# Kernel tuning notes

Measured on AMD Instinct MI355X. Metric: run time of the kernel, lower is better.

Reference implementation:

```python
import jax, jax.numpy as jnp
import numpy as np
from jax import lax

IOU_THRESHOLD = 0.5
CONF_THRESHOLD = 0.05
MAX_DETECTIONS = 100


def setup_inputs() -> dict:
    key = jax.random.key(0)
    k1, k2, k3 = jax.random.split(key, 3)
    B, N, C = 8, 100000, 80
    # xyxy boxes: top-left in [0,64), size in [16,128)
    xy = jax.random.uniform(k1, (B, N, 2), dtype=jnp.float32) * 64.0
    wh = jax.random.uniform(k2, (B, N, 2), dtype=jnp.float32) * 112.0 + 16.0
    box_prediction = jnp.concatenate([xy, xy + wh], axis=-1)
    # class logits (from_logits=True); scale so max softmax prob clears threshold
    class_prediction = jax.random.normal(k3, (B, N, C), dtype=jnp.float32) * 2.0
    return {"box_prediction": box_prediction, "class_prediction": class_prediction}


def _iou_one_vs_all(ref, boxes):
    # tf.image.non_max_suppression semantics: coords treated as corners
    # [a, b, c, d]; area = (c-a)*(d-b); iou=0 if either area <= 0.
    a_r, b_r, c_r, d_r = ref[0], ref[1], ref[2], ref[3]
    area_r = (c_r - a_r) * (d_r - b_r)
    area_b = (boxes[:, 2] - boxes[:, 0]) * (boxes[:, 3] - boxes[:, 1])
    ih = jnp.maximum(0.0, jnp.minimum(c_r, boxes[:, 2]) - jnp.maximum(a_r, boxes[:, 0]))
    iw = jnp.maximum(0.0, jnp.minimum(d_r, boxes[:, 3]) - jnp.maximum(b_r, boxes[:, 1]))
    inter = ih * iw
    union = area_r + area_b - inter
    ok = (area_r > 0) & (area_b > 0) & (union > 0)
    return jnp.where(ok, inter / jnp.where(ok, union, 1.0), 0.0)


def _nms_one(boxes, scores):
    # greedy NMS on a single image: boxes [N,4], scores [N]
    active0 = scores >= CONF_THRESHOLD

    def step(active, _):
        masked = jnp.where(active, scores, -jnp.inf)
        idx = jnp.argmax(masked)
        ok = active[idx]
        iou = _iou_one_vs_all(boxes[idx], boxes)
        active = active & (iou <= IOU_THRESHOLD)
        active = active.at[idx].set(False)
        return active, (idx, ok)

    _, (idxs, oks) = lax.scan(step, active0, None, length=MAX_DETECTIONS)
    return idxs, oks  # [M] int, [M] bool


def _forward(box_prediction, class_prediction):
    # convert_format xyxy -> xywh (x, y, w, h)
    x1, y1, x2, y2 = jnp.split(box_prediction, 4, axis=-1)
    boxes = jnp.concatenate([x1, y1, x2 - x1, y2 - y1], axis=-1)  # [B,N,4]
    cls_p = jax.nn.softmax(class_prediction, axis=-1)  # from_logits=True
    scores = jnp.max(cls_p, axis=-1)  # [B,N]
    idxs, oks = jax.vmap(_nms_one)(boxes, scores)  # [B,M], [B,M]
    boxes_sel = jnp.take_along_axis(boxes, idxs[:, :, None], axis=1)  # [B,M,4]
    cls_sel = jnp.take_along_axis(cls_p, idxs[:, :, None], axis=1)  # [B,M,C]
    boxes_out = jnp.where(oks[:, :, None], boxes_sel, 0.0)
    cls_out = jnp.where(oks[:, :, None], cls_sel, 0.0)
    return boxes_out, cls_out


def reference(box_prediction, class_prediction):
    boxes_out, cls_out = _forward(box_prediction, class_prediction)
    cls_idx = jnp.argmax(cls_out, axis=2)
    return boxes_out, cls_idx, cls_out
```

## Files before the change

kernel.cpp:

```cpp
#include <hip/hip_runtime.h>
#include <stdint.h>

#define BATCH 8
#define NCLS 80
#define MAXDET 100
#define CAP 512
#define NBINS 10240
#define TT 1024
#define TCHUNK 10
#define BASEKEY (0x3D4CCCCDu >> 12)

__global__ __launch_bounds__(256)
void scores_kernel(const float* __restrict__ cls,
                   float* __restrict__ scores, int BN) {
  int gid = blockIdx.x * 256 + threadIdx.x;
  int row = gid >> 1;
  int l = gid & 1;
  if (row >= BN) return;
  const float4* p4 = (const float4*)(cls + (size_t)row * NCLS);

  float4 v[10];
#pragma unroll
  for (int i = 0; i < 10; i++) v[i] = p4[l + 2 * i];

  float m = fmaxf(fmaxf(v[0].x, v[0].y), fmaxf(v[0].z, v[0].w));
#pragma unroll
  for (int i = 1; i < 10; i++)
    m = fmaxf(m, fmaxf(fmaxf(v[i].x, v[i].y), fmaxf(v[i].z, v[i].w)));
  m = fmaxf(m, __shfl_xor(m, 1));

  float a0 = 0.f, a1 = 0.f, a2 = 0.f, a3 = 0.f;
#pragma unroll
  for (int i = 0; i < 10; i++) {
    a0 += expf(v[i].x - m);
    a1 += expf(v[i].y - m);
    a2 += expf(v[i].z - m);
    a3 += expf(v[i].w - m);
  }
  float s_half = (a0 + a1) + (a2 + a3);
  float s = s_half + __shfl_xor(s_half, 1);
  if (l == 0) scores[row] = 1.0f / s;
}

__global__ __launch_bounds__(TT)
void tail_kernel(const float* __restrict__ box, const float* __restrict__ cls,
                 const float* __restrict__ scores,
                 float* __restrict__ out, int N) {
  __shared__ uint32_t lh[NBINS];
  __shared__ uint32_t chs[TT];
  __shared__ unsigned long long sk[CAP];
  __shared__ float sbox[CAP][4];
  __shared__ uint32_t sidx[CAP];
  __shared__ float4 accb[MAXDET];
  __shared__ float4 accp[MAXDET];
  __shared__ uint32_t pick_i[MAXDET];
  __shared__ int T_sh, nacc_sh;
  __shared__ uint32_t lctr;

  const int b = blockIdx.x;
  const int tid = threadIdx.x;
  const float* sc = scores + (size_t)b * N;

#pragma unroll
  for (int j = 0; j < TCHUNK; j++) lh[tid + j * TT] = 0;
  if (tid < CAP) sk[tid] = 0ULL;
  if (tid == 0) { lctr = 0; T_sh = NBINS; }
  __syncthreads();

  const float4* sc4 = (const float4*)sc;
  const int N4 = N >> 2;
  for (int i = tid; i < N4; i += TT) {
    float4 v = sc4[i];
    if (v.x >= 0.05f) atomicAdd(&lh[(__float_as_uint(v.x) >> 12) - BASEKEY], 1u);
    if (v.y >= 0.05f) atomicAdd(&lh[(__float_as_uint(v.y) >> 12) - BASEKEY], 1u);
    if (v.z >= 0.05f) atomicAdd(&lh[(__float_as_uint(v.z) >> 12) - BASEKEY], 1u);
    if (v.w >= 0.05f) atomicAdd(&lh[(__float_as_uint(v.w) >> 12) - BASEKEY], 1u);
  }
  for (int i = (N4 << 2) + tid; i < N; i += TT) {
    float s = sc[i];
    if (s >= 0.05f) atomicAdd(&lh[(__float_as_uint(s) >> 12) - BASEKEY], 1u);
  }
  __syncthreads();

  uint32_t csum = 0;
#pragma unroll
  for (int j = 0; j < TCHUNK; j++) csum += lh[tid * TCHUNK + j];
  chs[tid] = csum;
  __syncthreads();
  for (int off = 1; off < TT; off <<= 1) {
    uint32_t v = chs[tid];
    uint32_t add = (tid + off < TT) ? chs[tid + off] : 0u;
    __syncthreads();
    chs[tid] = v + add;
    __syncthreads();
  }
  {
    uint32_t St = chs[tid];
    uint32_t Sprev = (tid > 0) ? chs[tid - 1] : 0xFFFFFFFFu;
    if (St <= CAP && (tid == 0 || Sprev > CAP)) {
      int T = 0;
      if (tid != 0) {
        uint32_t cum = St;
        int lo = (tid - 1) * TCHUNK;
        T = lo;
        for (int bb = tid * TCHUNK - 1; bb >= lo; bb--) {
          uint32_t nb = cum + lh[bb];
          if (nb > CAP) { T = bb + 1; break; }
          cum = nb;
          if (bb == lo) T = lo;
        }
      }
      T_sh = T;
    }
  }
  __syncthreads();
  const uint32_t T = (uint32_t)T_sh;

  for (int i = tid; i < N4; i += TT) {
    float4 v = sc4[i];
#pragma unroll
    for (int c = 0; c < 4; c++) {
      float s = (c == 0) ? v.x : (c == 1) ? v.y : (c == 2) ? v.z : v.w;
      if (s >= 0.05f) {
        uint32_t key = (__float_as_uint(s) >> 12) - BASEKEY;
        if (key >= T) {
          uint32_t slot = atomicAdd(&lctr, 1u);
          if (slot < CAP)
            sk[slot] = ((unsigned long long)__float_as_uint(s) << 32) |
                       (unsigned long long)(~(uint32_t)(i * 4 + c));
        }
      }
    }
  }
  for (int i = (N4 << 2) + tid; i < N; i += TT) {
    float s = sc[i];
    if (s >= 0.05f) {
      uint32_t key = (__float_as_uint(s) >> 12) - BASEKEY;
      if (key >= T) {
        uint32_t slot = atomicAdd(&lctr, 1u);
        if (slot < CAP)
          sk[slot] = ((unsigned long long)__float_as_uint(s) << 32) |
                     (unsigned long long)(~(uint32_t)i);
      }
    }
  }
  __syncthreads();
  uint32_t nc = lctr; if (nc > CAP) nc = CAP;

  for (int k = 2; k <= CAP; k <<= 1) {
    for (int j = k >> 1; j > 0; j >>= 1) {
      int i = tid;
      if (i < CAP) {
        int ixj = i ^ j;
        if (ixj > i) {
          unsigned long long a = sk[i], c = sk[ixj];
          if (((i & k) == 0) ? (a < c) : (a > c)) { sk[i] = c; sk[ixj] = a; }
        }
      }
      __syncthreads();
    }
  }

  if (tid < CAP) {
    unsigned long long k = sk[tid];
    uint32_t idx = (uint32_t)k ^ 0xFFFFFFFFu;
    sidx[tid] = idx;
    if (k != 0ULL) {
      const float4 f = *(const float4*)(box + ((size_t)b * N + idx) * 4);
      sbox[tid][0] = f.x; sbox[tid][1] = f.y;
      sbox[tid][2] = f.z - f.x; sbox[tid][3] = f.w - f.y;
    } else {
      sbox[tid][0] = 0.f; sbox[tid][1] = 0.f; sbox[tid][2] = 0.f; sbox[tid][3] = 0.f;
    }
  }
  __syncthreads();

  if (tid < 64) {
    const int lane = tid;
    int nacc = 0, nprop = 0;
    for (int cursor = 0; cursor < (int)nc && nacc < MAXDET; cursor += 64) {
      const int c = cursor + lane;
      bool alive = (c < (int)nc);
      float c0 = 0.f, c1 = 0.f, c2 = 0.f, c3 = 0.f;
      uint32_t myidx = 0;
      if (alive) {
        c0 = sbox[c][0]; c1 = sbox[c][1]; c2 = sbox[c][2]; c3 = sbox[c][3];
        myidx = sidx[c];
      }
      const float area_b = (c2 - c0) * (c3 - c1);

#pragma unroll 2
      for (int a = 0; a < nprop; a++) {
        float4 ar = accp[a];
        float area_r = (ar.z - ar.x) * (ar.w - ar.y);
        float ih = fmaxf(0.f, fminf(ar.z, c2) - fmaxf(ar.x, c0));
        float iw = fmaxf(0.f, fminf(ar.w, c3) - fmaxf(ar.y, c1));
        float inter = ih * iw;
        float uni = area_r + area_b - inter;
        bool okk = (area_r > 0.f) && (area_b > 0.f) && (uni > 0.f);
        float iou = okk ? (inter / uni) : 0.f;
        if (iou > 0.5f) alive = false;
      }

      unsigned long long am = __ballot(alive);
      while (am != 0ULL && nacc < MAXDET) {
        int L = (int)(__ffsll(am) - 1);
        float r0 = __shfl(c0, L), r1 = __shfl(c1, L);
        float r2 = __shfl(c2, L), r3 = __shfl(c3, L);
        uint32_t ridx = (uint32_t)__shfl((int)myidx, L);
        bool proper = (r2 > r0) && (r3 > r1);
        if (lane == 0) {
          pick_i[nacc] = ridx;
          accb[nacc] = make_float4(r0, r1, r2, r3);
          if (proper) accp[nprop] = make_float4(r0, r1, r2, r3);
        }
        asm volatile("s_waitcnt lgkmcnt(0)" ::: "memory");
        if (lane == L) alive = false;
        if (proper) {
          if (alive) {
            float area_r = (r2 - r0) * (r3 - r1);
            float ih = fmaxf(0.f, fminf(r2, c2) - fmaxf(r0, c0));
            float iw = fmaxf(0.f, fminf(r3, c3) - fmaxf(r1, c1));
            float inter = ih * iw;
            float uni = area_r + area_b - inter;
            bool okk = (area_r > 0.f) && (area_b > 0.f) && (uni > 0.f);
            float iou = okk ? (inter / uni) : 0.f;
            if (iou > 0.5f) alive = false;
          }
          nprop++;
        }
        am = __ballot(alive);
        nacc++;
      }
    }
    if (lane == 0) nacc_sh = nacc;
  }
  __syncthreads();

  const int nacc = nacc_sh;
  if (tid >= MAXDET) return;
  const int r = b * MAXDET + tid;
  float* boxes_out  = out;
  float* clsidx_out = out + BATCH * MAXDET * 4;
  float* cls_out    = out + BATCH * MAXDET * 4 + BATCH * MAXDET;

  if (tid >= nacc) {
    boxes_out[r * 4 + 0] = 0.f; boxes_out[r * 4 + 1] = 0.f;
    boxes_out[r * 4 + 2] = 0.f; boxes_out[r * 4 + 3] = 0.f;
    clsidx_out[r] = 0.f;
    for (int j = 0; j < NCLS; j++) cls_out[r * NCLS + j] = 0.f;
    return;
  }
  float4 bb = accb[tid];
  boxes_out[r * 4 + 0] = bb.x;
  boxes_out[r * 4 + 1] = bb.y;
  boxes_out[r * 4 + 2] = bb.z;
  boxes_out[r * 4 + 3] = bb.w;

  uint32_t idx = pick_i[tid];
  const float4* p = (const float4*)(cls + ((size_t)b * N + idx) * NCLS);
  float x[NCLS];
#pragma unroll
  for (int i = 0; i < NCLS / 4; i++) {
    float4 v = p[i];
    x[4 * i] = v.x; x[4 * i + 1] = v.y; x[4 * i + 2] = v.z; x[4 * i + 3] = v.w;
  }
  float m = x[0];
#pragma unroll
  for (int i = 1; i < NCLS; i++) m = fmaxf(m, x[i]);
  float r8[8];
#pragma unroll
  for (int j = 0; j < 8; j++) r8[j] = 0.0f;
#pragma unroll
  for (int i = 0; i < NCLS / 8; i++)
#pragma unroll
    for (int j = 0; j < 8; j++) r8[j] += expf(x[i * 8 + j] - m);
  float s = ((r8[0] + r8[1]) + (r8[2] + r8[3])) + ((r8[4] + r8[5]) + (r8[6] + r8[7]));

  float best = -1.f; int bi = 0;
  for (int j = 0; j < NCLS; j++) {
    float pj = expf(x[j] - m) / s;
    cls_out[r * NCLS + j] = pj;
    if (pj > best) { best = pj; bi = j; }
  }
  clsidx_out[r] = (float)bi;
}

extern "C" void kernel_launch(void* const* d_in, const int* in_sizes, int n_in,
                              void* d_out, int out_size, void* d_ws, size_t ws_size,
                              hipStream_t stream) {
  (void)n_in; (void)out_size; (void)ws_size;
  const float* box = (const float*)d_in[0];
  const float* cls = (const float*)d_in[1];
  const int N = in_sizes[0] / (BATCH * 4);
  const int BN = BATCH * N;

  float* ws_scores = (float*)d_ws;

  {
    long long tot = (long long)BN * 2;
    int blocks = (int)((tot + 255) / 256);
    scores_kernel<<<blocks, 256, 0, stream>>>(cls, ws_scores, BN);
  }
  tail_kernel<<<BATCH, TT, 0, stream>>>(box, cls, ws_scores, (float*)d_out, N);
}
```

Measured before the change: 116.8 us.

## Stage class logits through LDS with coalesced wave loads in persistent scores kernel

```diff
diff --git a/kernel.cpp b/kernel.cpp
--- a/kernel.cpp
+++ b/kernel.cpp
@@ -10,36 +10,71 @@
 #define TCHUNK 10
 #define BASEKEY (0x3D4CCCCDu >> 12)
 
+#define SG_ROWS 32
+#define SG_PAD 84
+#define SG_WAVES 4
+#define SG_BLOCKS 768
+
 __global__ __launch_bounds__(256)
 void scores_kernel(const float* __restrict__ cls,
                    float* __restrict__ scores, int BN) {
-  int gid = blockIdx.x * 256 + threadIdx.x;
-  int row = gid >> 1;
-  int l = gid & 1;
-  if (row >= BN) return;
-  const float4* p4 = (const float4*)(cls + (size_t)row * NCLS);
-
-  float4 v[10];
-#pragma unroll
-  for (int i = 0; i < 10; i++) v[i] = p4[l + 2 * i];
-
-  float m = fmaxf(fmaxf(v[0].x, v[0].y), fmaxf(v[0].z, v[0].w));
-#pragma unroll
-  for (int i = 1; i < 10; i++)
-    m = fmaxf(m, fmaxf(fmaxf(v[i].x, v[i].y), fmaxf(v[i].z, v[i].w)));
-  m = fmaxf(m, __shfl_xor(m, 1));
-
-  float a0 = 0.f, a1 = 0.f, a2 = 0.f, a3 = 0.f;
-#pragma unroll
-  for (int i = 0; i < 10; i++) {
-    a0 += expf(v[i].x - m);
-    a1 += expf(v[i].y - m);
-    a2 += expf(v[i].z - m);
-    a3 += expf(v[i].w - m);
-  }
-  float s_half = (a0 + a1) + (a2 + a3);
-  float s = s_half + __shfl_xor(s_half, 1);
-  if (l == 0) scores[row] = 1.0f / s;
+  __shared__ float slab_all[SG_WAVES * SG_ROWS * SG_PAD];
+  const int lane = threadIdx.x & 63;
+  const int wid  = threadIdx.x >> 6;
+  float* slab = slab_all + wid * (SG_ROWS * SG_PAD);
+  const int ngroups = (BN + SG_ROWS - 1) / SG_ROWS;
+  const int wstride = gridDim.x * SG_WAVES;
+
+  for (int g = blockIdx.x * SG_WAVES + wid; g < ngroups; g += wstride) {
+    const int row0 = g * SG_ROWS;
+    int rows = BN - row0; if (rows > SG_ROWS) rows = SG_ROWS;
+    const int nf4 = rows * 20;
+    const float4* src = (const float4*)(cls + (size_t)row0 * NCLS);
+
+    float4 vr[10];
+#pragma unroll
+    for (int k = 0; k < 10; k++) {
+      int f = k * 64 + lane;
+      if (f < nf4) vr[k] = src[f];
+    }
+#pragma unroll
+    for (int k = 0; k < 10; k++) {
+      int f = k * 64 + lane;
+      if (f < nf4) {
+        int r = f / 20, p = f - r * 20;
+        *(float4*)&slab[r * SG_PAD + p * 4] = vr[k];
+      }
+    }
+    asm volatile("s_waitcnt lgkmcnt(0)" ::: "memory");
+
+    const int rt = lane >> 1;
+    const int l = lane & 1;
+    if (rt < rows) {
+      const float4* t4 = (const float4*)&slab[rt * SG_PAD];
+      float4 v[10];
+#pragma unroll
+      for (int i = 0; i < 10; i++) v[i] = t4[l + 2 * i];
+
+      float m = fmaxf(fmaxf(v[0].x, v[0].y), fmaxf(v[0].z, v[0].w));
+#pragma unroll
+      for (int i = 1; i < 10; i++)
+        m = fmaxf(m, fmaxf(fmaxf(v[i].x, v[i].y), fmaxf(v[i].z, v[i].w)));
+      m = fmaxf(m, __shfl_xor(m, 1));
+
+      float a0 = 0.f, a1 = 0.f, a2 = 0.f, a3 = 0.f;
+#pragma unroll
+      for (int i = 0; i < 10; i++) {
+        a0 += expf(v[i].x - m);
+        a1 += expf(v[i].y - m);
+        a2 += expf(v[i].z - m);
+        a3 += expf(v[i].w - m);
+      }
+      float s_half = (a0 + a1) + (a2 + a3);
+      float s = s_half + __shfl_xor(s_half, 1);
+      if (l == 0) scores[row0 + rt] = 1.0f / s;
+    }
+    asm volatile("s_waitcnt lgkmcnt(0)" ::: "memory");
+  }
 }
 
 __global__ __launch_bounds__(TT)
@@ -297,10 +332,6 @@
 
   float* ws_scores = (float*)d_ws;
 
-  {
-    long long tot = (long long)BN * 2;
-    int blocks = (int)((tot + 255) / 256);
-    scores_kernel<<<blocks, 256, 0, stream>>>(cls, ws_scores, BN);
-  }
+  scores_kernel<<<SG_BLOCKS, 256, 0, stream>>>(cls, ws_scores, BN);
   tail_kernel<<<BATCH, TT, 0, stream>>>(box, cls, ws_scores, (float*)d_out, N);
 }
```

New measurement: 223.3 us. 1.91x slower.

## Stage softmax-score rows through double-buffered LDS with persistent waves

Applied to the files above, without the earlier changes.

```diff
diff --git a/kernel.cpp b/kernel.cpp
--- a/kernel.cpp
+++ b/kernel.cpp
@@ -10,36 +10,91 @@
 #define TCHUNK 10
 #define BASEKEY (0x3D4CCCCDu >> 12)
 
-__global__ __launch_bounds__(256)
+#define PR_ROWS 32
+#define PR_PAD 84
+#define PR_WAVES 2
+#define PR_BLOCKS 768
+
+__global__ __launch_bounds__(128, 1)
 void scores_kernel(const float* __restrict__ cls,
                    float* __restrict__ scores, int BN) {
-  int gid = blockIdx.x * 256 + threadIdx.x;
-  int row = gid >> 1;
-  int l = gid & 1;
-  if (row >= BN) return;
-  const float4* p4 = (const float4*)(cls + (size_t)row * NCLS);
-
-  float4 v[10];
-#pragma unroll
-  for (int i = 0; i < 10; i++) v[i] = p4[l + 2 * i];
-
-  float m = fmaxf(fmaxf(v[0].x, v[0].y), fmaxf(v[0].z, v[0].w));
-#pragma unroll
-  for (int i = 1; i < 10; i++)
-    m = fmaxf(m, fmaxf(fmaxf(v[i].x, v[i].y), fmaxf(v[i].z, v[i].w)));
-  m = fmaxf(m, __shfl_xor(m, 1));
-
-  float a0 = 0.f, a1 = 0.f, a2 = 0.f, a3 = 0.f;
-#pragma unroll
-  for (int i = 0; i < 10; i++) {
-    a0 += expf(v[i].x - m);
-    a1 += expf(v[i].y - m);
-    a2 += expf(v[i].z - m);
-    a3 += expf(v[i].w - m);
-  }
-  float s_half = (a0 + a1) + (a2 + a3);
-  float s = s_half + __shfl_xor(s_half, 1);
-  if (l == 0) scores[row] = 1.0f / s;
+  __shared__ float slab_all[PR_WAVES * 2 * PR_ROWS * PR_PAD];
+  const int lane = threadIdx.x & 63;
+  const int wid  = threadIdx.x >> 6;
+  float* slabA = slab_all + (wid * 2 + 0) * (PR_ROWS * PR_PAD);
+  float* slabB = slab_all + (wid * 2 + 1) * (PR_ROWS * PR_PAD);
+  const int ngroups = (BN + PR_ROWS - 1) / PR_ROWS;
+  const int wstride = gridDim.x * PR_WAVES;
+
+  int g = blockIdx.x * PR_WAVES + wid;
+  if (g >= ngroups) return;
+
+  int rr[10], pp[10];
+#pragma unroll
+  for (int k = 0; k < 10; k++) {
+    int f = k * 64 + lane;
+    rr[k] = f / 20; pp[k] = (f - rr[k] * 20) * 4;
+  }
+
+  {
+    const float4* src = (const float4*)(cls + (size_t)g * PR_ROWS * NCLS);
+    float4 st[10];
+#pragma unroll
+    for (int k = 0; k < 10; k++) st[k] = src[k * 64 + lane];
+#pragma unroll
+    for (int k = 0; k < 10; k++) *(float4*)&slabA[rr[k] * PR_PAD + pp[k]] = st[k];
+  }
+
+  int cur = 0;
+  while (true) {
+    const int gn = g + wstride;
+
+    float4 st[10];
+    const bool have_next = (gn < ngroups);
+    if (have_next) {
+      const float4* srcn = (const float4*)(cls + (size_t)gn * PR_ROWS * NCLS);
+#pragma unroll
+      for (int k = 0; k < 10; k++) st[k] = srcn[k * 64 + lane];
+    }
+
+    {
+      float* slab = cur ? slabB : slabA;
+      const int rt = lane >> 1;
+      const int l = lane & 1;
+      const float4* t4 = (const float4*)&slab[rt * PR_PAD];
+      float4 v[10];
+#pragma unroll
+      for (int i = 0; i < 10; i++) v[i] = t4[l + 2 * i];
+
+      float m = fmaxf(fmaxf(v[0].x, v[0].y), fmaxf(v[0].z, v[0].w));
+#pragma unroll
+      for (int i = 1; i < 10; i++)
+        m = fmaxf(m, fmaxf(fmaxf(v[i].x, v[i].y), fmaxf(v[i].z, v[i].w)));
+      m = fmaxf(m, __shfl_xor(m, 1));
+
+      float a0 = 0.f, a1 = 0.f, a2 = 0.f, a3 = 0.f;
+#pragma unroll
+      for (int i = 0; i < 10; i++) {
+        a0 += expf(v[i].x - m);
+        a1 += expf(v[i].y - m);
+        a2 += expf(v[i].z - m);
+        a3 += expf(v[i].w - m);
+      }
+      float s_half = (a0 + a1) + (a2 + a3);
+      float s = s_half + __shfl_xor(s_half, 1);
+      if (l == 0) scores[g * PR_ROWS + rt] = 1.0f / s;
+    }
+
+    if (!have_next) break;
+
+    {
+      float* sl = cur ? slabA : slabB;
+#pragma unroll
+      for (int k = 0; k < 10; k++) *(float4*)&sl[rr[k] * PR_PAD + pp[k]] = st[k];
+    }
+    cur ^= 1;
+    g = gn;
+  }
 }
 
 __global__ __launch_bounds__(TT)
@@ -297,10 +352,6 @@
 
   float* ws_scores = (float*)d_ws;
 
-  {
-    long long tot = (long long)BN * 2;
-    int blocks = (int)((tot + 255) / 256);
-    scores_kernel<<<blocks, 256, 0, stream>>>(cls, ws_scores, BN);
-  }
+  scores_kernel<<<PR_BLOCKS, 128, 0, stream>>>(cls, ws_scores, BN);
   tail_kernel<<<BATCH, TT, 0, stream>>>(box, cls, ws_scores, (float*)d_out, N);
 }
```

Result: slower. 177.0 us (+51.5%).
